# Kernel optimization log

Measured on AMD Instinct MI355X. Metric: run time of the kernel, lower is better.

Reference implementation:

```python
import jax, jax.numpy as jnp
import numpy as np

B, A, C = 8, 150000, 10
ALPHA, GAMMA = 0.25, 2.0
STD = jnp.array([[0.1, 0.1, 0.2, 0.2]], dtype=jnp.float32)


def setup_inputs() -> dict:
    key = jax.random.key(0)
    ks = jax.random.split(key, 9)
    # ground-truth boxes (one per image), centered around (400,400)
    cx = jax.random.uniform(ks[0], (B,), minval=350., maxval=450.)
    cy = jax.random.uniform(ks[1], (B,), minval=350., maxval=450.)
    w = jax.random.uniform(ks[2], (B,), minval=80., maxval=180.)
    h = jax.random.uniform(ks[3], (B,), minval=80., maxval=180.)
    boxes = jnp.stack([cx - 0.5 * w, cy - 0.5 * h, cx + 0.5 * w, cy + 0.5 * h], axis=1)
    labels = (jax.random.uniform(ks[4], (B, C)) < 0.3).astype(jnp.float32)
    annotations = jnp.concatenate([boxes, labels], axis=1)  # [B, 4+C]
    n_near = A // 20
    kc = jax.random.split(ks[5], 4)
    ncx = jax.random.uniform(kc[0], (n_near,), minval=350., maxval=450.)
    ncy = jax.random.uniform(kc[1], (n_near,), minval=350., maxval=450.)
    nw = jax.random.uniform(kc[2], (n_near,), minval=80., maxval=180.)
    nh = jax.random.uniform(kc[3], (n_near,), minval=80., maxval=180.)
    kr = jax.random.split(ks[6], 4)
    rcx = jax.random.uniform(kr[0], (A - n_near,), minval=0., maxval=800.)
    rcy = jax.random.uniform(kr[1], (A - n_near,), minval=0., maxval=800.)
    rw = jax.random.uniform(kr[2], (A - n_near,), minval=20., maxval=300.)
    rh = jax.random.uniform(kr[3], (A - n_near,), minval=20., maxval=300.)
    acx = jnp.concatenate([ncx, rcx]); acy = jnp.concatenate([ncy, rcy])
    aw = jnp.concatenate([nw, rw]); ah = jnp.concatenate([nh, rh])
    anchors = jnp.stack([acx - 0.5 * aw, acy - 0.5 * ah, acx + 0.5 * aw, acy + 0.5 * ah], axis=1)[None]  # [1,A,4]
    attributes = jax.random.uniform(ks[7], (B, A, C), dtype=jnp.float32)  # probs in (0,1)
    regressions = jax.random.normal(ks[8], (B, A, 4), dtype=jnp.float32)
    return {"attributes": attributes, "regressions": regressions,
            "anchors": anchors, "annotations": annotations}


def reference(attributes, regressions, anchors, annotations):
    anchor = anchors[0]  # [A,4]
    aw = anchor[:, 2] - anchor[:, 0]
    ah = anchor[:, 3] - anchor[:, 1]
    acx = anchor[:, 0] + 0.5 * aw
    acy = anchor[:, 1] + 0.5 * ah

    def per_image(attribute, regression, ann):  # [A,C], [A,4], [4+C]
        box, labels = ann[:4], ann[4:]
        attribute = jnp.clip(attribute, 1e-4, 1.0 - 1e-4)
        # IoU of every anchor with the single gt box -> [A]
        area = (box[2] - box[0]) * (box[3] - box[1])
        iw = jnp.clip(jnp.minimum(anchor[:, 2], box[2]) - jnp.maximum(anchor[:, 0], box[0]), 0.0)
        ih = jnp.clip(jnp.minimum(anchor[:, 3], box[3]) - jnp.maximum(anchor[:, 1], box[1]), 0.0)
        inter = iw * ih
        union = jnp.clip(aw * ah + area - inter, 1e-8)
        iou = inter / union
        neg = iou < 0.4
        pos = iou >= 0.5
        num_pos = pos.sum()
        # classification targets: -1 ignore, 0 background, gt labels for positives
        targets = jnp.full(attribute.shape, -1.0, attribute.dtype)
        targets = jnp.where(neg[:, None], 0.0, targets)
        targets = jnp.where(pos[:, None], labels[None, :], targets)
        alpha_factor = jnp.where(targets == 1.0, ALPHA, 1.0 - ALPHA)
        focal_w = jnp.where(targets == 1.0, 1.0 - attribute, attribute)
        focal_w = alpha_factor * focal_w ** GAMMA
        bce = -(targets * jnp.log(attribute) + (1.0 - targets) * jnp.log(1.0 - attribute))
        att_loss = jnp.where(targets != -1.0, focal_w * bce, 0.0)
        att_loss = att_loss.sum() / jnp.maximum(num_pos.astype(attribute.dtype), 1.0)
        gw_raw = box[2] - box[0]; gh_raw = box[3] - box[1]
        gcx = box[0] + 0.5 * gw_raw; gcy = box[1] + 0.5 * gh_raw
        gw = jnp.clip(gw_raw, 1.0); gh = jnp.clip(gh_raw, 1.0)
        t = jnp.stack([(gcx - acx) / aw, (gcy - acy) / ah,
                       jnp.log(gw / aw), jnp.log(gh / ah)], axis=1) / STD  # [A,4]
        diff = jnp.abs(t - regression)
        rl = jnp.where(diff <= 1.0 / 9.0, 0.5 * 9.0 * diff ** 2, diff - 0.5 / 9.0)
        rl_sum = jnp.where(pos[:, None], rl, 0.0).sum()
        denom = jnp.maximum(num_pos, 1).astype(attribute.dtype) * 4.0  # mean over [P,4]
        reg_loss = jnp.where(num_pos > 0, rl_sum / denom, 0.0)
        return att_loss, reg_loss

    att_losses, reg_losses = jax.vmap(per_image)(attributes, regressions, annotations)
    return (att_losses.mean(keepdims=True), reg_losses.mean(keepdims=True))
```

## Files before the change

### kernel.cpp

```cpp
#include <hip/hip_runtime.h>

constexpr int B_IMG = 8;
constexpr int A_ANCH = 150000;
constexpr int C_CLS = 10;
constexpr int TPB = 256;
constexpr int NBX = (A_ANCH + TPB * 2 - 1) / (TPB * 2);

__global__ __launch_bounds__(TPB) void focal_main(
    const float* __restrict__ attr,
    const float* __restrict__ regr,
    const float* __restrict__ anch,
    const float* __restrict__ ann,
    float* __restrict__ att_part,
    float* __restrict__ rl_part,
    float* __restrict__ np_part)
{
    const int b = blockIdx.y;
    const int a0 = (blockIdx.x * TPB + threadIdx.x) * 2;
    const bool valid = (a0 < A_ANCH);

    float4 at4[5];
    float4 an4[2];
    if (valid) {
        const float4* ap = reinterpret_cast<const float4*>(attr + ((size_t)b * A_ANCH + a0) * C_CLS);
#pragma unroll
        for (int j = 0; j < 5; ++j) at4[j] = ap[j];
        const float4* anp = reinterpret_cast<const float4*>(anch) + a0;
        an4[0] = anp[0];
        an4[1] = anp[1];
    }

    const float* annb = ann + b * 14;
    const float bx0 = annb[0], by0 = annb[1], bx1 = annb[2], by1 = annb[3];
    float lab[C_CLS];
#pragma unroll
    for (int c = 0; c < C_CLS; ++c) lab[c] = annb[4 + c];

    const float gw_raw = bx1 - bx0;
    const float gh_raw = by1 - by0;
    const float area = gw_raw * gh_raw;
    const float gcx = bx0 + 0.5f * gw_raw;
    const float gcy = by0 + 0.5f * gh_raw;
    const float gw = fmaxf(gw_raw, 1.0f);
    const float gh = fmaxf(gh_raw, 1.0f);

    const float TH  = (float)(1.0 / 9.0);
    const float SUB = (float)(0.5 / 9.0);
    const float PHI = (float)(1.0 - 0.0001);

    float att_sum = 0.0f;
    float rl_sum = 0.0f;
    float npf = 0.0f;

    if (valid) {
        float av[20];
#pragma unroll
        for (int j = 0; j < 5; ++j) {
            av[4 * j + 0] = at4[j].x;
            av[4 * j + 1] = at4[j].y;
            av[4 * j + 2] = at4[j].z;
            av[4 * j + 3] = at4[j].w;
        }

#pragma unroll
        for (int k = 0; k < 2; ++k) {
            const float ax0 = an4[k].x, ay0 = an4[k].y, ax1 = an4[k].z, ay1 = an4[k].w;
            const float aw = ax1 - ax0;
            const float ah = ay1 - ay0;
            float iw = fminf(ax1, bx1) - fmaxf(ax0, bx0);
            float ih = fminf(ay1, by1) - fmaxf(ay0, by0);
            iw = fmaxf(iw, 0.0f);
            ih = fmaxf(ih, 0.0f);
            const float inter = iw * ih;
            const float uni = fmaxf(aw * ah + area - inter, 1e-8f);
            const float iou = inter / uni;
            const bool pos = (iou >= 0.5f);
            const bool neg = (iou < 0.4f);

            if (pos || neg) {
#pragma unroll
                for (int c = 0; c < C_CLS; ++c) {
                    float p = av[k * C_CLS + c];
                    p = fminf(fmaxf(p, 1e-4f), PHI);
                    const float tgt = pos ? lab[c] : 0.0f;
                    float loss;
                    if (tgt == 1.0f) {
                        const float q = 1.0f - p;
                        loss = 0.25f * (q * q) * (-__logf(p));
                    } else {
                        loss = 0.75f * (p * p) * (-__logf(1.0f - p));
                    }
                    att_sum += loss;
                }
            }
            if (pos) {
                npf += 1.0f;
                const float acx = ax0 + 0.5f * aw;
                const float acy = ay0 + 0.5f * ah;
                const float t0 = ((gcx - acx) / aw) / 0.1f;
                const float t1 = ((gcy - acy) / ah) / 0.1f;
                const float t2 = __logf(gw / aw) / 0.2f;
                const float t3 = __logf(gh / ah) / 0.2f;
                const float4 r = *reinterpret_cast<const float4*>(regr + ((size_t)b * A_ANCH + a0 + k) * 4);
                float d;
                d = fabsf(t0 - r.x); rl_sum += (d <= TH) ? 4.5f * d * d : d - SUB;
                d = fabsf(t1 - r.y); rl_sum += (d <= TH) ? 4.5f * d * d : d - SUB;
                d = fabsf(t2 - r.z); rl_sum += (d <= TH) ? 4.5f * d * d : d - SUB;
                d = fabsf(t3 - r.w); rl_sum += (d <= TH) ? 4.5f * d * d : d - SUB;
            }
        }
    }

#pragma unroll
    for (int off = 32; off > 0; off >>= 1) {
        att_sum += __shfl_down(att_sum, off);
        rl_sum  += __shfl_down(rl_sum, off);
        npf     += __shfl_down(npf, off);
    }

    __shared__ float s_att[TPB / 64];
    __shared__ float s_rl[TPB / 64];
    __shared__ float s_np[TPB / 64];
    const int wave = threadIdx.x >> 6;
    const int lane = threadIdx.x & 63;
    if (lane == 0) { s_att[wave] = att_sum; s_rl[wave] = rl_sum; s_np[wave] = npf; }
    __syncthreads();
    if (threadIdx.x == 0) {
        float a0s = 0.0f, r0 = 0.0f, n0 = 0.0f;
#pragma unroll
        for (int w = 0; w < TPB / 64; ++w) { a0s += s_att[w]; r0 += s_rl[w]; n0 += s_np[w]; }
        const int idx = b * NBX + blockIdx.x;
        att_part[idx] = a0s;
        rl_part[idx]  = r0;
        np_part[idx]  = n0;
    }
}

__global__ __launch_bounds__(512) void focal_finalize(
    const float* __restrict__ att_part,
    const float* __restrict__ rl_part,
    const float* __restrict__ np_part,
    float* __restrict__ out)
{
    const int wave = threadIdx.x >> 6;
    const int lane = threadIdx.x & 63;
    float as = 0.0f, rs = 0.0f, ns = 0.0f;
    if (wave < B_IMG) {
        for (int i = lane; i < NBX; i += 64) {
            as += att_part[wave * NBX + i];
            rs += rl_part[wave * NBX + i];
            ns += np_part[wave * NBX + i];
        }
    }
#pragma unroll
    for (int off = 32; off > 0; off >>= 1) {
        as += __shfl_down(as, off);
        rs += __shfl_down(rs, off);
        ns += __shfl_down(ns, off);
    }
    __shared__ float sa[B_IMG], sr[B_IMG], sn[B_IMG];
    if (lane == 0 && wave < B_IMG) { sa[wave] = as; sr[wave] = rs; sn[wave] = ns; }
    __syncthreads();
    if (threadIdx.x == 0) {
        double am = 0.0, rm = 0.0;
        for (int b = 0; b < B_IMG; ++b) {
            const double npd = (double)sn[b];
            const double npf = npd > 0.0 ? npd : 1.0;
            am += (double)sa[b] / npf;
            if (npd > 0.0) rm += (double)sr[b] / (npf * 4.0);
        }
        out[0] = (float)(am / (double)B_IMG);
        out[1] = (float)(rm / (double)B_IMG);
    }
}

extern "C" void kernel_launch(void* const* d_in, const int* in_sizes, int n_in,
                              void* d_out, int out_size, void* d_ws, size_t ws_size,
                              hipStream_t stream) {
    const float* attr = (const float*)d_in[0];
    const float* regr = (const float*)d_in[1];
    const float* anch = (const float*)d_in[2];
    const float* ann  = (const float*)d_in[3];
    float* out = (float*)d_out;

    float* att_part = (float*)d_ws;
    float* rl_part  = att_part + B_IMG * NBX;
    float* np_part  = rl_part + B_IMG * NBX;

    dim3 grid(NBX, B_IMG);
    focal_main<<<grid, TPB, 0, stream>>>(attr, regr, anch, ann, att_part, rl_part, np_part);
    focal_finalize<<<1, 512, 0, stream>>>(att_part, rl_part, np_part, out);
}
```

Baseline: 23.27 us.

## Coalesce attribute loads across block and share anchor flags via LDS

Attribute loads change from a per-thread contiguous 40-float chunk, which is strided across lanes, to block-wide coalesced float4 loads. Each anchor's pos/neg/ignore flag is computed once and published in shared memory, and each element looks up its anchor flag to compute focal loss. Labels are packed into a bitmask. The change is meant to improve memory coalescing on the dominant attribute stream. In exchange it adds a __syncthreads, an LDS lookup per element and integer division math, and it changes the order of the float sums.

```diff
diff --git a/kernel.cpp b/kernel.cpp
--- a/kernel.cpp
+++ b/kernel.cpp
@@ -4,7 +4,10 @@
 constexpr int A_ANCH = 150000;
 constexpr int C_CLS = 10;
 constexpr int TPB = 256;
-constexpr int NBX = (A_ANCH + TPB * 2 - 1) / (TPB * 2);
+constexpr int BA = TPB * 2;
+constexpr int NBX = (A_ANCH + BA - 1) / BA;
+constexpr int F4_PER_IMG = A_ANCH * C_CLS / 4;
+constexpr int F4_PER_BLK = BA * C_CLS / 4;
 
 __global__ __launch_bounds__(TPB) void focal_main(
     const float* __restrict__ attr,
@@ -15,26 +18,33 @@
     float* __restrict__ rl_part,
     float* __restrict__ np_part)
 {
-    const int b = blockIdx.y;
-    const int a0 = (blockIdx.x * TPB + threadIdx.x) * 2;
-    const bool valid = (a0 < A_ANCH);
-
-    float4 at4[5];
-    float4 an4[2];
-    if (valid) {
-        const float4* ap = reinterpret_cast<const float4*>(attr + ((size_t)b * A_ANCH + a0) * C_CLS);
-#pragma unroll
-        for (int j = 0; j < 5; ++j) at4[j] = ap[j];
-        const float4* anp = reinterpret_cast<const float4*>(anch) + a0;
-        an4[0] = anp[0];
-        an4[1] = anp[1];
-    }
+    __shared__ unsigned char sFlag[BA];
+
+    const int b   = blockIdx.y;
+    const int blk = blockIdx.x;
+    const int tid = threadIdx.x;
+
+    const float4* atp = reinterpret_cast<const float4*>(attr) + (size_t)b * F4_PER_IMG;
+    float4 av[5];
+#pragma unroll
+    for (int j = 0; j < 5; ++j) {
+        int f4 = blk * F4_PER_BLK + j * TPB + tid;
+        f4 = (f4 < F4_PER_IMG) ? f4 : (F4_PER_IMG - 1);
+        av[j] = atp[f4];
+    }
+    const int A0 = blk * BA + tid;
+    const int A1 = A0 + TPB;
+    const bool v0 = (A0 < A_ANCH);
+    const bool v1 = (A1 < A_ANCH);
+    const float4* anp = reinterpret_cast<const float4*>(anch);
+    const float4 an0 = anp[v0 ? A0 : 0];
+    const float4 an1 = anp[v1 ? A1 : 0];
 
     const float* annb = ann + b * 14;
     const float bx0 = annb[0], by0 = annb[1], bx1 = annb[2], by1 = annb[3];
-    float lab[C_CLS];
-#pragma unroll
-    for (int c = 0; c < C_CLS; ++c) lab[c] = annb[4 + c];
+    unsigned labmask = 0;
+#pragma unroll
+    for (int c = 0; c < C_CLS; ++c) labmask |= (annb[4 + c] == 1.0f ? 1u : 0u) << c;
 
     const float gw_raw = bx1 - bx0;
     const float gh_raw = by1 - by0;
@@ -52,61 +62,68 @@
     float rl_sum = 0.0f;
     float npf = 0.0f;
 
-    if (valid) {
-        float av[20];
-#pragma unroll
-        for (int j = 0; j < 5; ++j) {
-            av[4 * j + 0] = at4[j].x;
-            av[4 * j + 1] = at4[j].y;
-            av[4 * j + 2] = at4[j].z;
-            av[4 * j + 3] = at4[j].w;
-        }
-
+    {
+        const float4 anv[2] = {an0, an1};
+        const bool   val[2] = {v0, v1};
+        const int    aix[2] = {A0, A1};
+        unsigned flg[2] = {0u, 0u};
 #pragma unroll
         for (int k = 0; k < 2; ++k) {
-            const float ax0 = an4[k].x, ay0 = an4[k].y, ax1 = an4[k].z, ay1 = an4[k].w;
-            const float aw = ax1 - ax0;
-            const float ah = ay1 - ay0;
-            float iw = fminf(ax1, bx1) - fmaxf(ax0, bx0);
-            float ih = fminf(ay1, by1) - fmaxf(ay0, by0);
-            iw = fmaxf(iw, 0.0f);
-            ih = fmaxf(ih, 0.0f);
-            const float inter = iw * ih;
-            const float uni = fmaxf(aw * ah + area - inter, 1e-8f);
-            const float iou = inter / uni;
-            const bool pos = (iou >= 0.5f);
-            const bool neg = (iou < 0.4f);
-
-            if (pos || neg) {
-#pragma unroll
-                for (int c = 0; c < C_CLS; ++c) {
-                    float p = av[k * C_CLS + c];
-                    p = fminf(fmaxf(p, 1e-4f), PHI);
-                    const float tgt = pos ? lab[c] : 0.0f;
-                    float loss;
-                    if (tgt == 1.0f) {
-                        const float q = 1.0f - p;
-                        loss = 0.25f * (q * q) * (-__logf(p));
-                    } else {
-                        loss = 0.75f * (p * p) * (-__logf(1.0f - p));
-                    }
-                    att_sum += loss;
+            if (val[k]) {
+                const float aw = anv[k].z - anv[k].x;
+                const float ah = anv[k].w - anv[k].y;
+                const float iw = fmaxf(fminf(anv[k].z, bx1) - fmaxf(anv[k].x, bx0), 0.0f);
+                const float ih = fmaxf(fminf(anv[k].w, by1) - fmaxf(anv[k].y, by0), 0.0f);
+                const float inter = iw * ih;
+                const float uni = fmaxf(aw * ah + area - inter, 1e-8f);
+                const float iou = inter / uni;
+                const bool pos = (iou >= 0.5f);
+                const bool neg = (iou < 0.4f);
+                flg[k] = pos ? 2u : (neg ? 1u : 0u);
+                if (pos) {
+                    npf += 1.0f;
+                    const float acx = anv[k].x + 0.5f * aw;
+                    const float acy = anv[k].y + 0.5f * ah;
+                    const float t0 = ((gcx - acx) / aw) / 0.1f;
+                    const float t1 = ((gcy - acy) / ah) / 0.1f;
+                    const float t2 = __logf(gw / aw) / 0.2f;
+                    const float t3 = __logf(gh / ah) / 0.2f;
+                    const float4 r = *reinterpret_cast<const float4*>(
+                        regr + ((size_t)b * A_ANCH + aix[k]) * 4);
+                    float d;
+                    d = fabsf(t0 - r.x); rl_sum += (d <= TH) ? 4.5f * d * d : d - SUB;
+                    d = fabsf(t1 - r.y); rl_sum += (d <= TH) ? 4.5f * d * d : d - SUB;
+                    d = fabsf(t2 - r.z); rl_sum += (d <= TH) ? 4.5f * d * d : d - SUB;
+                    d = fabsf(t3 - r.w); rl_sum += (d <= TH) ? 4.5f * d * d : d - SUB;
                 }
             }
-            if (pos) {
-                npf += 1.0f;
-                const float acx = ax0 + 0.5f * aw;
-                const float acy = ay0 + 0.5f * ah;
-                const float t0 = ((gcx - acx) / aw) / 0.1f;
-                const float t1 = ((gcy - acy) / ah) / 0.1f;
-                const float t2 = __logf(gw / aw) / 0.2f;
-                const float t3 = __logf(gh / ah) / 0.2f;
-                const float4 r = *reinterpret_cast<const float4*>(regr + ((size_t)b * A_ANCH + a0 + k) * 4);
-                float d;
-                d = fabsf(t0 - r.x); rl_sum += (d <= TH) ? 4.5f * d * d : d - SUB;
-                d = fabsf(t1 - r.y); rl_sum += (d <= TH) ? 4.5f * d * d : d - SUB;
-                d = fabsf(t2 - r.z); rl_sum += (d <= TH) ? 4.5f * d * d : d - SUB;
-                d = fabsf(t3 - r.w); rl_sum += (d <= TH) ? 4.5f * d * d : d - SUB;
+        }
+        sFlag[tid]       = (unsigned char)flg[0];
+        sFlag[tid + TPB] = (unsigned char)flg[1];
+    }
+    __syncthreads();
+
+#pragma unroll
+    for (int j = 0; j < 5; ++j) {
+        const int l0 = j * (TPB * 4) + tid * 4;
+        const float pv[4] = {av[j].x, av[j].y, av[j].z, av[j].w};
+#pragma unroll
+        for (int d = 0; d < 4; ++d) {
+            const int l = l0 + d;
+            const int a = (l * 6554) >> 16;
+            const int c = l - a * 10;
+            const unsigned flag = sFlag[a];
+            if (flag) {
+                const float p = fminf(fmaxf(pv[d], 1e-4f), PHI);
+                const bool t1 = (flag == 2u) && ((labmask >> c) & 1u);
+                float loss;
+                if (t1) {
+                    const float q = 1.0f - p;
+                    loss = 0.25f * q * q * (-__logf(p));
+                } else {
+                    loss = 0.75f * p * p * (-__logf(1.0f - p));
+                }
+                att_sum += loss;
             }
         }
     }
@@ -121,15 +138,15 @@
     __shared__ float s_att[TPB / 64];
     __shared__ float s_rl[TPB / 64];
     __shared__ float s_np[TPB / 64];
-    const int wave = threadIdx.x >> 6;
-    const int lane = threadIdx.x & 63;
+    const int wave = tid >> 6;
+    const int lane = tid & 63;
     if (lane == 0) { s_att[wave] = att_sum; s_rl[wave] = rl_sum; s_np[wave] = npf; }
     __syncthreads();
-    if (threadIdx.x == 0) {
+    if (tid == 0) {
         float a0s = 0.0f, r0 = 0.0f, n0 = 0.0f;
 #pragma unroll
         for (int w = 0; w < TPB / 64; ++w) { a0s += s_att[w]; r0 += s_rl[w]; n0 += s_np[w]; }
-        const int idx = b * NBX + blockIdx.x;
+        const int idx = b * NBX + blk;
         att_part[idx] = a0s;
         rl_part[idx]  = r0;
         np_part[idx]  = n0;
@@ -165,9 +182,9 @@
         double am = 0.0, rm = 0.0;
         for (int b = 0; b < B_IMG; ++b) {
             const double npd = (double)sn[b];
-            const double npf = npd > 0.0 ? npd : 1.0;
-            am += (double)sa[b] / npf;
-            if (npd > 0.0) rm += (double)sr[b] / (npf * 4.0);
+            const double den = npd > 0.0 ? npd : 1.0;
+            am += (double)sa[b] / den;
+            if (npd > 0.0) rm += (double)sr[b] / (den * 4.0);
         }
         out[0] = (float)(am / (double)B_IMG);
         out[1] = (float)(rm / (double)B_IMG);
```

New measurement: 27.15 us. +16.7%, slower.
